# Kernel optimization log

Hardware: AMD Instinct MI355X
Metric: run time of the kernel (lower is better)

The kernel has to match this reference:

```python
import jax, jax.numpy as jnp
import numpy as np

VOCAB = 30001
EMB = 256
HID = 512          # bidirectional total; 256 per direction
NTAG = 9
B, L = 64, 512


def setup_inputs() -> dict:
    key = jax.random.key(0)
    ks = jax.random.split(key, 12)
    Hd = HID // 2
    s = 0.1
    return {
        "x": jax.random.randint(ks[0], (B, L), 0, VOCAB),
        "embed": jax.random.normal(ks[1], (VOCAB, EMB), jnp.float32) * s,
        "W_ih_f": jax.random.normal(ks[2], (4 * Hd, EMB), jnp.float32) * s,
        "W_hh_f": jax.random.normal(ks[3], (4 * Hd, Hd), jnp.float32) * s,
        "b_f": jax.random.normal(ks[4], (4 * Hd,), jnp.float32) * s,
        "W_ih_b": jax.random.normal(ks[5], (4 * Hd, EMB), jnp.float32) * s,
        "W_hh_b": jax.random.normal(ks[6], (4 * Hd, Hd), jnp.float32) * s,
        "b_b": jax.random.normal(ks[7], (4 * Hd,), jnp.float32) * s,
        "W_out": jax.random.normal(ks[8], (NTAG, HID), jnp.float32) * s,
        "b_out": jax.random.normal(ks[9], (NTAG,), jnp.float32) * s,
        "start_trans": jax.random.normal(ks[10], (NTAG,), jnp.float32) * s,
        "trans": jax.random.normal(ks[11], (NTAG, NTAG), jnp.float32) * s,
        "end_trans": jax.random.normal(jax.random.fold_in(key, 99), (NTAG,), jnp.float32) * s,
    }


def _lstm_dir(xg, W_hh, reverse):
    # xg: [L, B, 4H] precomputed input-to-gate projections (+ bias)
    Hd = W_hh.shape[1]
    nB = xg.shape[1]
    h0 = jnp.zeros((nB, Hd), xg.dtype)
    c0 = jnp.zeros((nB, Hd), xg.dtype)

    def step(carry, gx):
        h, c = carry
        g = gx + h @ W_hh.T                     # [B, 4H]
        i, f, gg, o = jnp.split(g, 4, axis=-1)  # torch gate order i,f,g,o
        c = jax.nn.sigmoid(f) * c + jax.nn.sigmoid(i) * jnp.tanh(gg)
        h = jax.nn.sigmoid(o) * jnp.tanh(c)
        return (h, c), h

    _, hs = jax.lax.scan(step, (h0, c0), xg, reverse=reverse)
    return hs  # [L, B, H]


def _viterbi(emissions, start, trans, end):
    # emissions: [L, B, T]. Max-plus DP (torchcrf CRF.decode, no mask).
    score0 = start + emissions[0]  # [B, T]

    def step(score, em_t):
        # score[b, i] + trans[i, j] + em_t[b, j]
        nxt = score[:, :, None] + trans[None] + em_t[:, None, :]
        return jnp.max(nxt, axis=1), jnp.argmax(nxt, axis=1)

    score, history = jax.lax.scan(step, score0, emissions[1:])  # history: [L-1, B, T]
    score = score + end
    last = jnp.argmax(score, axis=-1)   # [B] best tag at position L-1
    best = jnp.max(score, axis=-1)      # [B] best path score

    def back(tag, idx_t):
        prev = jnp.take_along_axis(idx_t, tag[:, None], axis=1)[:, 0]
        return prev, prev

    _, tags_head = jax.lax.scan(back, last, history, reverse=True)  # [L-1, B]
    tags = jnp.concatenate([tags_head, last[None]], axis=0)         # [L, B]
    return tags.T, best


def reference(x, embed, W_ih_f, W_hh_f, b_f, W_ih_b, W_hh_b, b_b,
              W_out, b_out, start_trans, trans, end_trans):
    xt = x.T                              # [L, B] time-first
    emb = embed[xt]                       # [L, B, E]
    gx_f = jnp.einsum('lbe,ge->lbg', emb, W_ih_f) + b_f
    gx_b = jnp.einsum('lbe,ge->lbg', emb, W_ih_b) + b_b
    hf = _lstm_dir(gx_f, W_hh_f, reverse=False)
    hb = _lstm_dir(gx_b, W_hh_b, reverse=True)
    outputs = jnp.concatenate([hf, hb], axis=-1)            # [L, B, HID]
    emissions = jnp.einsum('lbh,th->lbt', outputs, W_out) + b_out  # [L, B, T]
    tags, best = _viterbi(emissions, start_trans, trans, end_trans)
    return tags, best
```

## Files before the change

kernel.cpp:

```cpp
#include <hip/hip_runtime.h>
#include <math.h>


#define Bv 64
#define Lv 512

__device__ __forceinline__ float sigmoidf_(float x) { return 1.0f / (1.0f + expf(-x)); }

__global__ __launch_bounds__(256, 1) void lstm_persist(
    const int* __restrict__ x, const float* __restrict__ embed,
    const float* __restrict__ Wih_f, const float* __restrict__ Whh_f, const float* __restrict__ bf,
    const float* __restrict__ Wih_b, const float* __restrict__ Whh_b, const float* __restrict__ bb_,
    float* __restrict__ h_glob, int* __restrict__ cnts, float* __restrict__ h_hist)
{
    const int bid = blockIdx.x;
    const int d  = bid >> 7;
    const int ug = (bid >> 2) & 31;
    const int bg = bid & 3;
    const int tid = threadIdx.x;
    const int u0 = ug * 8;
    const int b0 = bg * 16;

    const float* Wih  = d ? Wih_b : Wih_f;
    const float* Whh  = d ? Whh_b : Whh_f;
    const float* bias = d ? bb_   : bf;

    const int ks = tid >> 5;
    const int tr = (tid >> 2) & 7;
    const int tb = tid & 3;
    const int k0 = ks * 32;

    __shared__ float wih_lds[32][260];
    __shared__ float h_lds[16][260];
    __shared__ float emb_lds[2][16][260];
    __shared__ float parts[4][32][16];
    __shared__ float gates[32][16];
    __shared__ float bias_lds[32];

    {
        const int row = tid >> 3;
        const int seg = tid & 7;
        const int g = row >> 3, j = row & 7;
        const float4* src = reinterpret_cast<const float4*>(
            Wih + ((size_t)(g * 256 + u0 + j)) * 256 + seg * 32);
        float4* dst = reinterpret_cast<float4*>(&wih_lds[row][seg * 32]);
        #pragma unroll
        for (int q = 0; q < 8; ++q) dst[q] = src[q];
    }
    if (tid < 32) bias_lds[tid] = bias[(tid >> 3) * 256 + u0 + (tid & 7)];

    float4 whh[4][8];
    #pragma unroll
    for (int i = 0; i < 4; ++i) {
        const float* wr = Whh + ((size_t)(i * 256 + u0 + tr)) * 256 + k0;
        #pragma unroll
        for (int m = 0; m < 8; ++m) whh[i][m] = *reinterpret_cast<const float4*>(wr + 4 * m);
    }

    float creg = 0.f;
    int* cnt_ptr = cnts + (d * 4 + bg) * 32;

    {
        const int b = tid >> 4;
        const int cseg = tid & 15;
        const int t_eff0 = d ? (Lv - 1) : 0;
        const int xv = x[(b0 + b) * Lv + t_eff0];
        const float4* src = reinterpret_cast<const float4*>(embed + (size_t)xv * 256 + cseg * 16);
        float4* dstp = reinterpret_cast<float4*>(&emb_lds[0][b][cseg * 16]);
        dstp[0] = src[0]; dstp[1] = src[1]; dstp[2] = src[2]; dstp[3] = src[3];
    }
    __syncthreads();

    for (int tt = 0; tt < Lv; ++tt) {
        const int par = tt & 1;

        float acc[4][4];
        #pragma unroll
        for (int i = 0; i < 4; ++i)
            #pragma unroll
            for (int u = 0; u < 4; ++u) acc[i][u] = 0.f;

        #pragma unroll
        for (int m = 0; m < 8; ++m) {
            float4 ev[4];
            #pragma unroll
            for (int u = 0; u < 4; ++u)
                ev[u] = *reinterpret_cast<const float4*>(&emb_lds[par][tb + 4 * u][k0 + 4 * m]);
            #pragma unroll
            for (int i = 0; i < 4; ++i) {
                float4 wv = *reinterpret_cast<const float4*>(&wih_lds[tr + 8 * i][k0 + 4 * m]);
                #pragma unroll
                for (int u = 0; u < 4; ++u)
                    acc[i][u] += wv.x * ev[u].x + wv.y * ev[u].y + wv.z * ev[u].z + wv.w * ev[u].w;
            }
        }

        if (tt + 1 < Lv) {
            const int b = tid >> 4;
            const int cseg = tid & 15;
            const int t_eff1 = d ? (Lv - 2 - tt) : (tt + 1);
            const int xv = x[(b0 + b) * Lv + t_eff1];
            const float4* src = reinterpret_cast<const float4*>(embed + (size_t)xv * 256 + cseg * 16);
            float4 e0 = src[0], e1 = src[1], e2 = src[2], e3 = src[3];
            float4* dstp = reinterpret_cast<float4*>(&emb_lds[par ^ 1][b][cseg * 16]);
            dstp[0] = e0; dstp[1] = e1; dstp[2] = e2; dstp[3] = e3;
        }

        if (tid == 0 && tt > 0) {
            const int target = 32 * tt;
            int it = 0, v;
            for (;;) {
                asm volatile("global_load_dword %0, %1, off sc0 sc1\n\t"
                             "s_waitcnt vmcnt(0)"
                             : "=v"(v) : "v"(cnt_ptr) : "memory");
                if (v >= target) break;
                __builtin_amdgcn_s_sleep(1);
                if (++it > (1 << 24)) break;
            }
        }
        __syncthreads();

        if (tt > 0) {
            const float* hs = h_glob + ((size_t)par * 8 + d * 4 + bg) * 4096 + tid * 16;
            float4 a0, a1, a2, a3;
            asm volatile(
                "global_load_dwordx4 %0, %4, off sc0 sc1\n\t"
                "global_load_dwordx4 %1, %4, off offset:16 sc0 sc1\n\t"
                "global_load_dwordx4 %2, %4, off offset:32 sc0 sc1\n\t"
                "global_load_dwordx4 %3, %4, off offset:48 sc0 sc1\n\t"
                "s_waitcnt vmcnt(0)"
                : "=v"(a0), "=v"(a1), "=v"(a2), "=v"(a3)
                : "v"(hs) : "memory");
            __builtin_amdgcn_sched_barrier(0);
            const int u = tid;
            h_lds[ 0][u] = a0.x; h_lds[ 1][u] = a0.y; h_lds[ 2][u] = a0.z; h_lds[ 3][u] = a0.w;
            h_lds[ 4][u] = a1.x; h_lds[ 5][u] = a1.y; h_lds[ 6][u] = a1.z; h_lds[ 7][u] = a1.w;
            h_lds[ 8][u] = a2.x; h_lds[ 9][u] = a2.y; h_lds[10][u] = a2.z; h_lds[11][u] = a2.w;
            h_lds[12][u] = a3.x; h_lds[13][u] = a3.y; h_lds[14][u] = a3.z; h_lds[15][u] = a3.w;
        }
        __syncthreads();

        if (tt > 0) {
            #pragma unroll
            for (int m = 0; m < 8; ++m) {
                float4 hv[4];
                #pragma unroll
                for (int u = 0; u < 4; ++u)
                    hv[u] = *reinterpret_cast<const float4*>(&h_lds[tb + 4 * u][k0 + 4 * m]);
                #pragma unroll
                for (int i = 0; i < 4; ++i) {
                    float4 wv = whh[i][m];
                    #pragma unroll
                    for (int u = 0; u < 4; ++u)
                        acc[i][u] += wv.x * hv[u].x + wv.y * hv[u].y + wv.z * hv[u].z + wv.w * hv[u].w;
                }
            }
        }

        #pragma unroll
        for (int i = 0; i < 4; ++i)
            #pragma unroll
            for (int u = 0; u < 4; ++u)
                acc[i][u] += __shfl_xor(acc[i][u], 32);
        if ((tid & 32) == 0) {
            const int w = tid >> 6;
            #pragma unroll
            for (int i = 0; i < 4; ++i)
                #pragma unroll
                for (int u = 0; u < 4; ++u)
                    parts[w][tr + 8 * i][tb + 4 * u] = acc[i][u];
        }
        __syncthreads();
        #pragma unroll
        for (int half = 0; half < 2; ++half) {
            const int o = tid + half * 256;
            const int r = o >> 4, b = o & 15;
            gates[r][b] = parts[0][r][b] + parts[1][r][b] + parts[2][r][b] + parts[3][r][b]
                        + bias_lds[r];
        }
        __syncthreads();

        if (tid < 128) {
            const int j  = tid & 7;
            const int bb = tid >> 3;
            const int t_eff = d ? (Lv - 1 - tt) : tt;
            const float gi = gates[     j][bb];
            const float gf = gates[ 8 + j][bb];
            const float gg = gates[16 + j][bb];
            const float go = gates[24 + j][bb];
            creg = sigmoidf_(gf) * creg + sigmoidf_(gi) * tanhf(gg);
            const float h = sigmoidf_(go) * tanhf(creg);
            float* dst = h_glob + ((size_t)(par ^ 1) * 8 + d * 4 + bg) * 4096
                       + (size_t)(u0 + j) * 16 + bb;
            asm volatile("global_store_dword %0, %1, off sc0 sc1"
                         :: "v"(dst), "v"(h) : "memory");
            h_hist[((size_t)(b0 + bb) * Lv + t_eff) * 512 + d * 256 + u0 + j] = h;
        }
        asm volatile("s_waitcnt vmcnt(0)" ::: "memory");
        __syncthreads();
        if (tid == 0)
            __hip_atomic_fetch_add(cnt_ptr, 1, __ATOMIC_RELAXED, __HIP_MEMORY_SCOPE_AGENT);
    }
}

__global__ __launch_bounds__(256) void emis_kernel(
    const float* __restrict__ h_hist, const float* __restrict__ Wout,
    const float* __restrict__ bout, float* __restrict__ em)
{
    const int l  = blockIdx.x >> 2;
    const int bg = blockIdx.x & 3;
    const int tid = threadIdx.x;
    __shared__ float w_lds[9][516];
    __shared__ float h_ldsx[16][512];

    for (int i = tid; i < 9 * 512; i += 256) w_lds[i >> 9][i & 511] = Wout[i];
    for (int i = tid; i < 16 * 128; i += 256) {
        const int bb = i >> 7; const int k = (i & 127) * 4;
        *reinterpret_cast<float4*>(&h_ldsx[bb][k]) =
            *reinterpret_cast<const float4*>(&h_hist[((size_t)(bg * 16 + bb) * 512 + l) * 512 + k]);
    }
    __syncthreads();

    const int bb = tid >> 4;
    const int j = tid & 15;
    if (j < 9) {
        float acc = bout[j];
        #pragma unroll 4
        for (int k = 0; k < 512; k += 4) {
            float4 hv = *reinterpret_cast<const float4*>(&h_ldsx[bb][k]);
            float4 wv = *reinterpret_cast<const float4*>(&w_lds[j][k]);
            acc += hv.x * wv.x + hv.y * wv.y + hv.z * wv.z + hv.w * wv.w;
        }
        em[((size_t)l * 64 + bg * 16 + bb) * 9 + j] = acc;
    }
}

__global__ __launch_bounds__(576) void viterbi_fwd(
    const float* __restrict__ em, const float* __restrict__ start,
    const float* __restrict__ trans, const float* __restrict__ endt,
    unsigned char* __restrict__ hist, int* __restrict__ last_tag,
    float* __restrict__ out_best)
{
    const int tid = threadIdx.x;
    const int b = tid / 9;
    const int j = tid - b * 9;
    __shared__ float sc[2][64][9];
    float t9[9];
    #pragma unroll
    for (int i = 0; i < 9; ++i) t9[i] = trans[i * 9 + j];

    sc[0][b][j] = start[j] + em[tid];
    float emv = em[(64 + b) * 9 + j];
    __syncthreads();
    for (int t = 1; t < 512; ++t) {
        float em_nxt = (t < 511) ? em[((t + 1) * 64 + b) * 9 + j] : 0.f;
        const int cur = t & 1, prv = cur ^ 1;
        float best = -1e30f; int arg = 0;
        #pragma unroll
        for (int i = 0; i < 9; ++i) {
            float v = sc[prv][b][i] + t9[i];
            if (v > best) { best = v; arg = i; }
        }
        best += emv;
        sc[cur][b][j] = best;
        hist[((size_t)b * 512 + t) * 9 + j] = (unsigned char)arg;
        __syncthreads();
        emv = em_nxt;
    }
    sc[1][b][j] += endt[j];
    __syncthreads();
    if (j == 0) {
        float best = -1e30f; int arg = 0;
        #pragma unroll
        for (int i = 0; i < 9; ++i) {
            float v = sc[1][b][i];
            if (v > best) { best = v; arg = i; }
        }
        out_best[b] = best;
        last_tag[b] = arg;
    }
}

__global__ __launch_bounds__(256) void backtrack(
    const unsigned char* __restrict__ hist, const int* __restrict__ last_tag,
    float* __restrict__ out_tags)
{
    const int b = blockIdx.x;
    const int tid = threadIdx.x;
    __shared__ __align__(16) unsigned char hl[512 * 9];
    const uint4* src = reinterpret_cast<const uint4*>(hist + (size_t)b * 512 * 9);
    uint4* dst = reinterpret_cast<uint4*>(hl);
    for (int i = tid; i < 512 * 9 / 16; i += 256) dst[i] = src[i];
    __syncthreads();
    if (tid == 0) {
        int tag = last_tag[b];
        out_tags[b * 512 + 511] = (float)tag;
        for (int t = 511; t >= 1; --t) {
            tag = hl[t * 9 + tag];
            out_tags[b * 512 + t - 1] = (float)tag;
        }
    }
}

extern "C" void kernel_launch(void* const* d_in, const int* in_sizes, int n_in,
                              void* d_out, int out_size, void* d_ws, size_t ws_size,
                              hipStream_t stream)
{
    const int*   x     = (const int*)d_in[0];
    const float* embed = (const float*)d_in[1];
    const float* Wih_f = (const float*)d_in[2];
    const float* Whh_f = (const float*)d_in[3];
    const float* bf    = (const float*)d_in[4];
    const float* Wih_b = (const float*)d_in[5];
    const float* Whh_b = (const float*)d_in[6];
    const float* bb    = (const float*)d_in[7];
    const float* Wout  = (const float*)d_in[8];
    const float* bout  = (const float*)d_in[9];
    const float* start = (const float*)d_in[10];
    const float* trans = (const float*)d_in[11];
    const float* endt  = (const float*)d_in[12];

    char* ws = (char*)d_ws;
    float* h_glob = (float*)ws;
    int*   cnts   = (int*)(ws + 262144);
    float* h_hist = (float*)(ws + 266240);
    float* em     = (float*)(ws + 266240 + 67108864);
    int*   last_tag = (int*)(ws + 67375104 + 1179648);
    unsigned char* hist = (unsigned char*)(ws + 68554752 + 256);

    float* out = (float*)d_out;

    hipMemsetAsync(cnts, 0, 4096, stream);

    lstm_persist<<<256, 256, 0, stream>>>(x, embed, Wih_f, Whh_f, bf,
                                          Wih_b, Whh_b, bb,
                                          h_glob, cnts, h_hist);
    emis_kernel<<<2048, 256, 0, stream>>>(h_hist, Wout, bout, em);
    viterbi_fwd<<<1, 576, 0, stream>>>(em, start, trans, endt, hist, last_tag, out + 64 * 512);
    backtrack<<<64, 256, 0, stream>>>(hist, last_tag, out);
}
```

Baseline: 3.121 ms.

## Replace atomic counter barrier with per-producer flags and fold gate reduction

```diff
diff --git a/kernel.cpp b/kernel.cpp
--- a/kernel.cpp
+++ b/kernel.cpp
@@ -11,12 +11,13 @@
     const int* __restrict__ x, const float* __restrict__ embed,
     const float* __restrict__ Wih_f, const float* __restrict__ Whh_f, const float* __restrict__ bf,
     const float* __restrict__ Wih_b, const float* __restrict__ Whh_b, const float* __restrict__ bb_,
-    float* __restrict__ h_glob, int* __restrict__ cnts, float* __restrict__ h_hist)
+    float* __restrict__ h_glob, int* __restrict__ tags, float* __restrict__ h_hist)
 {
     const int bid = blockIdx.x;
     const int d  = bid >> 7;
     const int ug = (bid >> 2) & 31;
     const int bg = bid & 3;
+    const int g  = d * 4 + bg;
     const int tid = threadIdx.x;
     const int u0 = ug * 8;
     const int b0 = bg * 16;
@@ -33,16 +34,15 @@
     __shared__ float wih_lds[32][260];
     __shared__ float h_lds[16][260];
     __shared__ float emb_lds[2][16][260];
-    __shared__ float parts[4][32][16];
-    __shared__ float gates[32][16];
+    __shared__ float parts[4][32][17];
     __shared__ float bias_lds[32];
 
     {
         const int row = tid >> 3;
         const int seg = tid & 7;
-        const int g = row >> 3, j = row & 7;
+        const int gq = row >> 3, j = row & 7;
         const float4* src = reinterpret_cast<const float4*>(
-            Wih + ((size_t)(g * 256 + u0 + j)) * 256 + seg * 32);
+            Wih + ((size_t)(gq * 256 + u0 + j)) * 256 + seg * 32);
         float4* dst = reinterpret_cast<float4*>(&wih_lds[row][seg * 32]);
         #pragma unroll
         for (int q = 0; q < 8; ++q) dst[q] = src[q];
@@ -58,7 +58,8 @@
     }
 
     float creg = 0.f;
-    int* cnt_ptr = cnts + (d * 4 + bg) * 32;
+    const int* my_tag = tags + g * 32 + (tid >> 3);
+    int* rel_tag = tags + g * 32 + ug;
 
     {
         const int b = tid >> 4;
@@ -106,22 +107,16 @@
             dstp[0] = e0; dstp[1] = e1; dstp[2] = e2; dstp[3] = e3;
         }
 
-        if (tid == 0 && tt > 0) {
-            const int target = 32 * tt;
-            int it = 0, v;
+        if (tt > 0) {
+            int v, it = 0;
             for (;;) {
                 asm volatile("global_load_dword %0, %1, off sc0 sc1\n\t"
                              "s_waitcnt vmcnt(0)"
-                             : "=v"(v) : "v"(cnt_ptr) : "memory");
-                if (v >= target) break;
-                __builtin_amdgcn_s_sleep(1);
-                if (++it > (1 << 24)) break;
+                             : "=v"(v) : "v"(my_tag) : "memory");
+                if (v >= tt) break;
+                if (++it > (1 << 22)) break;
             }
-        }
-        __syncthreads();
-
-        if (tt > 0) {
-            const float* hs = h_glob + ((size_t)par * 8 + d * 4 + bg) * 4096 + tid * 16;
+            const float* hs = h_glob + ((size_t)par * 8 + g) * 4096 + tid * 16;
             float4 a0, a1, a2, a3;
             asm volatile(
                 "global_load_dwordx4 %0, %4, off sc0 sc1\n\t"
@@ -171,26 +166,21 @@
                     parts[w][tr + 8 * i][tb + 4 * u] = acc[i][u];
         }
         __syncthreads();
-        #pragma unroll
-        for (int half = 0; half < 2; ++half) {
-            const int o = tid + half * 256;
-            const int r = o >> 4, b = o & 15;
-            gates[r][b] = parts[0][r][b] + parts[1][r][b] + parts[2][r][b] + parts[3][r][b]
-                        + bias_lds[r];
-        }
-        __syncthreads();
 
         if (tid < 128) {
             const int j  = tid & 7;
             const int bb = tid >> 3;
             const int t_eff = d ? (Lv - 1 - tt) : tt;
-            const float gi = gates[     j][bb];
-            const float gf = gates[ 8 + j][bb];
-            const float gg = gates[16 + j][bb];
-            const float go = gates[24 + j][bb];
-            creg = sigmoidf_(gf) * creg + sigmoidf_(gi) * tanhf(gg);
-            const float h = sigmoidf_(go) * tanhf(creg);
-            float* dst = h_glob + ((size_t)(par ^ 1) * 8 + d * 4 + bg) * 4096
+            float gv[4];
+            #pragma unroll
+            for (int q = 0; q < 4; ++q) {
+                const int r = q * 8 + j;
+                gv[q] = parts[0][r][bb] + parts[1][r][bb] + parts[2][r][bb] + parts[3][r][bb]
+                      + bias_lds[r];
+            }
+            creg = sigmoidf_(gv[1]) * creg + sigmoidf_(gv[0]) * tanhf(gv[2]);
+            const float h = sigmoidf_(gv[3]) * tanhf(creg);
+            float* dst = h_glob + ((size_t)(par ^ 1) * 8 + g) * 4096
                        + (size_t)(u0 + j) * 16 + bb;
             asm volatile("global_store_dword %0, %1, off sc0 sc1"
                          :: "v"(dst), "v"(h) : "memory");
@@ -198,8 +188,11 @@
         }
         asm volatile("s_waitcnt vmcnt(0)" ::: "memory");
         __syncthreads();
-        if (tid == 0)
-            __hip_atomic_fetch_add(cnt_ptr, 1, __ATOMIC_RELAXED, __HIP_MEMORY_SCOPE_AGENT);
+        if (tid == 0) {
+            int val = tt + 1;
+            asm volatile("global_store_dword %0, %1, off sc0 sc1"
+                         :: "v"(rel_tag), "v"(val) : "memory");
+        }
     }
 }
 
@@ -322,7 +315,7 @@
 
     char* ws = (char*)d_ws;
     float* h_glob = (float*)ws;
-    int*   cnts   = (int*)(ws + 262144);
+    int*   tags   = (int*)(ws + 262144);
     float* h_hist = (float*)(ws + 266240);
     float* em     = (float*)(ws + 266240 + 67108864);
     int*   last_tag = (int*)(ws + 67375104 + 1179648);
@@ -330,11 +323,11 @@
 
     float* out = (float*)d_out;
 
-    hipMemsetAsync(cnts, 0, 4096, stream);
+    hipMemsetAsync(tags, 0, 4096, stream);
 
     lstm_persist<<<256, 256, 0, stream>>>(x, embed, Wih_f, Whh_f, bf,
                                           Wih_b, Whh_b, bb,
-                                          h_glob, cnts, h_hist);
+                                          h_glob, tags, h_hist);
     emis_kernel<<<2048, 256, 0, stream>>>(h_hist, Wout, bout, em);
     viterbi_fwd<<<1, 576, 0, stream>>>(em, start, trans, endt, hist, last_tag, out + 64 * 512);
     backtrack<<<64, 256, 0, stream>>>(hist, last_tag, out);
```

Measured after the change: 2.852 ms. -8.6%, faster.
